# Kernel optimization log

Measured on AMD Instinct MI355X. Metric: run time of the kernel, lower is better.

The kernel has to match this reference:

```python
import jax, jax.numpy as jnp
import numpy as np
from jax import lax

B, CIN, COUT, H, W = 4, 256, 256, 64, 64
K = 3  # kernel size
PAD = 1
STRIDE = 1


def setup_inputs() -> dict:
    key = jax.random.key(0)
    k1, k2, k3, k4 = jax.random.split(key, 4)
    x = jax.random.normal(k1, (B, CIN, H, W), dtype=jnp.float32)
    # small offset weights so learned offsets are modest (original init is zeros)
    offset_w = jax.random.normal(k2, (3 * K * K, CIN, K, K), dtype=jnp.float32) * 0.01
    offset_b = jax.random.normal(k3, (3 * K * K,), dtype=jnp.float32) * 0.01
    dcn_w = jax.random.normal(k4, (COUT, CIN, K, K), dtype=jnp.float32) * (1.0 / np.sqrt(CIN * K * K))
    return {"x": x, "offset_w": offset_w, "offset_b": offset_b, "dcn_w": dcn_w}


def _dcnv2(x, offset_w, offset_b, dcn_w):
    b, c, h, w = x.shape
    kk = K * K
    # offset conv (standard 3x3, stride 1, pad 1)
    o = lax.conv_general_dilated(
        x, offset_w, (STRIDE, STRIDE), ((PAD, PAD), (PAD, PAD)),
        dimension_numbers=("NCHW", "OIHW", "NCHW"))
    o = o + offset_b[None, :, None, None]
    ho, wo = o.shape[2], o.shape[3]
    off = o[:, : 2 * kk].reshape(b, kk, 2, ho, wo)  # pairs are (dy, dx)
    dy, dx = off[:, :, 0], off[:, :, 1]             # [b,kk,ho,wo]
    mask = jax.nn.sigmoid(o[:, 2 * kk:])            # [b,kk,ho,wo]

    ki, kj = jnp.meshgrid(jnp.arange(K), jnp.arange(K), indexing="ij")
    ki = ki.reshape(kk).astype(jnp.float32)
    kj = kj.reshape(kk).astype(jnp.float32)
    base_y = (jnp.arange(ho, dtype=jnp.float32) * STRIDE - PAD)[None, None, :, None] + ki[None, :, None, None]
    base_x = (jnp.arange(wo, dtype=jnp.float32) * STRIDE - PAD)[None, None, None, :] + kj[None, :, None, None]
    py = base_y + dy  # [b,kk,ho,wo] sampling y
    px = base_x + dx  # sampling x

    y0 = jnp.floor(py)
    x0 = jnp.floor(px)
    wy = py - y0  # bilinear fractional weights
    wx = px - x0
    y0i = y0.astype(jnp.int32)
    x0i = x0.astype(jnp.int32)

    xT = x.transpose(0, 2, 3, 1)  # [b,h,w,c] for channel-last gathers
    bidx = jnp.arange(b)[:, None, None, None]

    def gather(yi, xi):
        # zero padding outside the image
        valid = (yi >= 0) & (yi < h) & (xi >= 0) & (xi < w)
        yc = jnp.clip(yi, 0, h - 1)
        xc = jnp.clip(xi, 0, w - 1)
        v = xT[bidx, yc, xc]  # [b,kk,ho,wo,c]
        return v * valid[..., None].astype(x.dtype)

    g00 = gather(y0i, x0i)
    g01 = gather(y0i, x0i + 1)
    g10 = gather(y0i + 1, x0i)
    g11 = gather(y0i + 1, x0i + 1)

    wy_ = wy[..., None]
    wx_ = wx[..., None]
    sampled = (g00 * (1 - wy_) * (1 - wx_) + g01 * (1 - wy_) * wx_
               + g10 * wy_ * (1 - wx_) + g11 * wy_ * wx_)
    sampled = sampled * mask[..., None]  # modulation

    wk = dcn_w.reshape(dcn_w.shape[0], c, kk)  # [o,c,kk]
    return jnp.einsum("bkhwc,ock->bohw", sampled, wk)


def reference(x, offset_w, offset_b, dcn_w):
    return _dcnv2(x, offset_w, offset_b, dcn_w)
```

## Files before the change

kernel.cpp:

```cpp
#include <hip/hip_runtime.h>
#include <hip/hip_bf16.h>
#include <stdint.h>
#include <math.h>

#define KDIM 2304

typedef __attribute__((ext_vector_type(8))) short bf16x8;
typedef __attribute__((ext_vector_type(4))) float f32x4;

__device__ inline unsigned short f2bf(float f) {
  union { float f; unsigned int u; } v; v.f = f;
  unsigned int u = v.u;
  unsigned int r = (u + 0x7FFFu + ((u >> 16) & 1u)) >> 16;
  return (unsigned short)r;
}
__device__ inline float bf2f(unsigned short h) {
  union { unsigned int u; float f; } v; v.u = ((unsigned int)h) << 16;
  return v.f;
}

__device__ inline void gl2lds16(const void* g, void* l) {
  __builtin_amdgcn_global_load_lds((const __attribute__((address_space(1))) void*)g,
                                   (__attribute__((address_space(3))) void*)l,
                                   16, 0, 0);
}

__global__ __launch_bounds__(256) void k_transpose(const float* __restrict__ x,
                                                   unsigned short* __restrict__ xTb) {
  __shared__ float tile[32][33];
  int t = threadIdx.x;
  int tx = t & 31, ty = t >> 5;
  int p0 = blockIdx.x * 32;
  int c0 = blockIdx.y * 32;
  int b  = blockIdx.z;
  const float* xb = x + ((size_t)b << 20);
#pragma unroll
  for (int i = 0; i < 4; ++i) {
    int c = c0 + ty + i * 8;
    tile[ty + i * 8][tx] = xb[((size_t)c << 12) + p0 + tx];
  }
  __syncthreads();
  unsigned short* ob = xTb + ((size_t)b << 20);
#pragma unroll
  for (int i = 0; i < 4; ++i) {
    int p = p0 + ty + i * 8;
    ob[(((size_t)p) << 8) + c0 + tx] = f2bf(tile[tx][ty + i * 8]);
  }
}

__global__ __launch_bounds__(256) void k_wprep(const float* __restrict__ dcn_w,
                                               const float* __restrict__ offset_w,
                                               unsigned short* __restrict__ Wpk,
                                               unsigned short* __restrict__ Wob,
                                               unsigned short* __restrict__ zp) {
  int gid = blockIdx.x * 256 + threadIdx.x;
  const int N1 = 72 * 8192;
  const int N2 = 32 * KDIM;
  if (gid < N1) {
    int j = gid & 7;
    int lane = (gid >> 3) & 63;
    int mb = (gid >> 9) & 15;
    int kc = gid >> 13;
    int row = mb * 16 + (lane & 15);
    int gk = kc * 32 + ((lane >> 4) << 3) + j;
    int c = gk & 255, kidx = gk >> 8;
    Wpk[gid] = f2bf(dcn_w[((size_t)(row * 256 + c)) * 9 + kidx]);
  } else if (gid < N1 + N2) {
    int g = gid - N1;
    int ch = g / KDIM, k = g % KDIM;
    int kidx = k >> 8, c = k & 255;
    Wob[g] = (ch < 27) ? f2bf(offset_w[((size_t)(ch * 256 + c)) * 9 + kidx])
                       : (unsigned short)0;
  } else if (gid < N1 + N2 + 128) {
    zp[gid - N1 - N2] = 0;
  }
}

__global__ __launch_bounds__(256) void k_offs_gemm(const unsigned short* __restrict__ xTb,
                                                   const unsigned short* __restrict__ Wob,
                                                   const unsigned short* __restrict__ zp,
                                                   float* __restrict__ O2p) {
  __shared__ unsigned short As[2][64 * 32];
  __shared__ unsigned short Bs[2][32 * 32];
  int t = threadIdx.x;
  int wv = t >> 6, lane = t & 63;
  int n0 = blockIdx.x * 64;
  int z = blockIdx.y;
  int r0 = t >> 2, coff = (t & 3) * 8;

  int rowA = n0 + r0;
  int b_ = rowA >> 12, hw = rowA & 4095, h = hw >> 6, w = hw & 63;

  f32x4 acc[2] = {};

  auto stage = [&](int kt, int buf) {
    int k0 = kt * 32;
    int kidx = k0 >> 8, c0 = k0 & 255;
    int di = kidx / 3 - 1, dj = kidx % 3 - 1;
    int y = h + di, xx = w + dj;
    const unsigned short* g = (y >= 0 && y < 64 && xx >= 0 && xx < 64)
        ? xTb + (((((size_t)b_) << 12) + (y << 6) + xx) << 8) + c0 + coff
        : zp;
    gl2lds16(g, (char*)As[buf] + wv * 1024);
    if (t < 128) {
      const unsigned short* gB = Wob + (size_t)(t >> 2) * KDIM + k0 + coff;
      gl2lds16(gB, (char*)Bs[buf] + wv * 1024);
    }
  };

  int kbeg = z * 36, kend = kbeg + 36;
  stage(kbeg, 0);

  for (int kt = kbeg; kt < kend; ++kt) {
    int buf = (kt - kbeg) & 1;
    if (kt + 1 < kend) {
      stage(kt + 1, buf ^ 1);
      if (wv < 2) asm volatile("s_waitcnt vmcnt(2)" ::: "memory");
      else        asm volatile("s_waitcnt vmcnt(1)" ::: "memory");
    } else {
      asm volatile("s_waitcnt vmcnt(0)" ::: "memory");
    }
    asm volatile("s_barrier" ::: "memory");

    bf16x8 aF, bF[2];
    aF = *(const bf16x8*)(As[buf] + (wv * 16 + (lane & 15)) * 32 + (lane >> 4) * 8);
#pragma unroll
    for (int j = 0; j < 2; ++j)
      bF[j] = *(const bf16x8*)(Bs[buf] + (j * 16 + (lane & 15)) * 32 + (lane >> 4) * 8);
#pragma unroll
    for (int j = 0; j < 2; ++j)
      acc[j] = __builtin_amdgcn_mfma_f32_16x16x32_bf16(aF, bF[j], acc[j], 0, 0, 0);

    asm volatile("s_barrier" ::: "memory");
  }

  int quad = lane >> 4, cl = lane & 15;
  float* O2z = O2p + (size_t)z * 16384 * 32;
#pragma unroll
  for (int j = 0; j < 2; ++j) {
    int col = j * 16 + cl;
#pragma unroll
    for (int r = 0; r < 4; ++r) {
      int row = n0 + wv * 16 + quad * 4 + r;
      O2z[(size_t)row * 32 + col] = acc[j][r];
    }
  }
}

__global__ __launch_bounds__(256) void k_sweights(const float* __restrict__ O2p,
                                                  const float* __restrict__ offb,
                                                  float* __restrict__ SW) {
  int gid = blockIdx.x * 256 + threadIdx.x;
  if (gid >= 9 * 16384) return;
  int k = gid >> 14;
  int bhw = gid & 16383;
  int h = (bhw >> 6) & 63, w = bhw & 63;

  const float* o0 = O2p + (size_t)bhw * 32;
  const float* o1 = o0 + (size_t)16384 * 32;
  float dy = o0[2 * k]     + o1[2 * k]     + offb[2 * k];
  float dx = o0[2 * k + 1] + o1[2 * k + 1] + offb[2 * k + 1];
  float mv = o0[18 + k]    + o1[18 + k]    + offb[18 + k];
  float mask = 1.0f / (1.0f + expf(-mv));

  float py = (float)(h - 1 + k / 3) + dy;
  float px = (float)(w - 1 + k % 3) + dx;
  float y0f = floorf(py), x0f = floorf(px);
  float wy = py - y0f, wx = px - x0f;
  int y0 = (int)y0f, x0 = (int)x0f;
  int y1 = y0 + 1, x1 = x0 + 1;

  float vy0 = (y0 >= 0 && y0 < 64) ? 1.f : 0.f;
  float vy1 = (y1 >= 0 && y1 < 64) ? 1.f : 0.f;
  float vx0 = (x0 >= 0 && x0 < 64) ? 1.f : 0.f;
  float vx1 = (x1 >= 0 && x1 < 64) ? 1.f : 0.f;
  int y0c = min(max(y0, 0), 63), y1c = min(max(y1, 0), 63);
  int x0c = min(max(x0, 0), 63), x1c = min(max(x1, 0), 63);

  float4 wv4;
  wv4.x = (1.f - wy) * (1.f - wx) * vy0 * vx0 * mask;
  wv4.y = (1.f - wy) * wx * vy0 * vx1 * mask;
  wv4.z = wy * (1.f - wx) * vy1 * vx0 * mask;
  wv4.w = wy * wx * vy1 * vx1 * mask;
  uint4 ov;
  ov.x = (unsigned)(((y0c << 6) + x0c) << 8);
  ov.y = (unsigned)(((y0c << 6) + x1c) << 8);
  ov.z = (unsigned)(((y1c << 6) + x0c) << 8);
  ov.w = (unsigned)(((y1c << 6) + x1c) << 8);

  float* p = SW + (size_t)gid * 8;
  *(float4*)p = wv4;
  *(uint4*)(p + 4) = ov;
}

__global__ __launch_bounds__(512) void k_fused(const unsigned short* __restrict__ Wpk,
                                               const unsigned short* __restrict__ xTb,
                                               const float* __restrict__ SW,
                                               float* __restrict__ out) {
  __shared__ __align__(16) unsigned short Bs[2][64 * 40];
  int t = threadIdx.x;
  int wv = t >> 6, lane = t & 63;
  int wm = wv & 3, wn = wv >> 2;
  int n0 = blockIdx.x * 64;
  int b  = n0 >> 12;
  const unsigned short* xb = xTb + ((size_t)b << 20);

  int r = t >> 3, g = t & 7;
  int ch0 = g * 4;
  int bsw = r * 40 + ch0;

  const unsigned short* wpBase = Wpk + ((size_t)(wm * 4 * 64 + lane)) * 8;

  f32x4 acc[4][2] = {};

  float4 wv4; uint4 ov;
  {
    const float* sw = SW + ((size_t)(n0 + r)) * 8;
    wv4 = *(const float4*)sw;
    ov  = *(const uint4*)(sw + 4);
  }
  float4 wv4n = wv4; uint4 ovn = ov;
  ushort4 q00, q01, q10, q11;
  bf16x8 aF[4], aFn[4];

  {
    unsigned c = (unsigned)ch0;
    q00 = *(const ushort4*)(xb + ov.x + c);
    q01 = *(const ushort4*)(xb + ov.y + c);
    q10 = *(const ushort4*)(xb + ov.z + c);
    q11 = *(const ushort4*)(xb + ov.w + c);
#pragma unroll
    for (int i = 0; i < 4; ++i)
      aF[i] = *(const bf16x8*)(wpBase + (size_t)i * 512);
  }

#pragma unroll 2
  for (int kt = 0; kt < 72; ++kt) {
    float s[4];
    s[0] = wv4.x * bf2f(q00.x) + wv4.y * bf2f(q01.x) + wv4.z * bf2f(q10.x) + wv4.w * bf2f(q11.x);
    s[1] = wv4.x * bf2f(q00.y) + wv4.y * bf2f(q01.y) + wv4.z * bf2f(q10.y) + wv4.w * bf2f(q11.y);
    s[2] = wv4.x * bf2f(q00.z) + wv4.y * bf2f(q01.z) + wv4.z * bf2f(q10.z) + wv4.w * bf2f(q11.z);
    s[3] = wv4.x * bf2f(q00.w) + wv4.y * bf2f(q01.w) + wv4.z * bf2f(q10.w) + wv4.w * bf2f(q11.w);
    union { __hip_bfloat162 h2[2]; ushort4 v; } pk;
    pk.h2[0] = __float22bfloat162_rn(make_float2(s[0], s[1]));
    pk.h2[1] = __float22bfloat162_rn(make_float2(s[2], s[3]));
    *(ushort4*)(&Bs[kt & 1][bsw]) = pk.v;

    if ((kt & 7) == 0 && kt < 64) {
      const float* swp = SW + ((size_t)((((kt >> 3) + 1) << 14) + n0 + r)) * 8;
      wv4n = *(const float4*)swp;
      ovn  = *(const uint4*)(swp + 4);
    }

    if (kt < 71) {
      int kn = kt + 1;
      if ((kn & 7) == 0) { wv4 = wv4n; ov = ovn; }
      unsigned c = (unsigned)(((kn & 7) << 5) + ch0);
      q00 = *(const ushort4*)(xb + ov.x + c);
      q01 = *(const ushort4*)(xb + ov.y + c);
      q10 = *(const ushort4*)(xb + ov.z + c);
      q11 = *(const ushort4*)(xb + ov.w + c);
#pragma unroll
      for (int i = 0; i < 4; ++i)
        aFn[i] = *(const bf16x8*)(wpBase + ((size_t)kn * 16 + i) * 512);
    }

    asm volatile("s_waitcnt lgkmcnt(0)\n\ts_barrier" ::: "memory");

    bf16x8 bF[2];
#pragma unroll
    for (int j = 0; j < 2; ++j)
      bF[j] = *(const bf16x8*)(&Bs[kt & 1][(wn * 32 + j * 16 + (lane & 15)) * 40 + (lane >> 4) * 8]);
#pragma unroll
    for (int i = 0; i < 4; ++i)
#pragma unroll
      for (int j = 0; j < 2; ++j)
        acc[i][j] = __builtin_amdgcn_mfma_f32_16x16x32_bf16(aF[i], bF[j], acc[i][j], 0, 0, 0);
    if (kt < 71) {
#pragma unroll
      for (int i = 0; i < 4; ++i) aF[i] = aFn[i];
    }
  }

  int quad = lane >> 4, cl = lane & 15;
  float* ob = out + (((size_t)b) << 20);
#pragma unroll
  for (int i = 0; i < 4; ++i) {
    int mbase = wm * 64 + i * 16 + quad * 4;
#pragma unroll
    for (int j = 0; j < 2; ++j) {
      int hw = (n0 & 4095) + wn * 32 + j * 16 + cl;
      float* op = ob + hw;
#pragma unroll
      for (int rr = 0; rr < 4; ++rr)
        op[((size_t)(mbase + rr)) << 12] = acc[i][j][rr];
    }
  }
}

extern "C" void kernel_launch(void* const* d_in, const int* in_sizes, int n_in,
                              void* d_out, int out_size, void* d_ws, size_t ws_size,
                              hipStream_t stream) {
  const float* x        = (const float*)d_in[0];
  const float* offset_w = (const float*)d_in[1];
  const float* offset_b = (const float*)d_in[2];
  const float* dcn_w    = (const float*)d_in[3];
  float* out = (float*)d_out;

  char* ws = (char*)d_ws;
  size_t off = 0;
  auto carve = [&](size_t bytes) -> void* {
    void* p = ws + off;
    off += (bytes + 255) & ~(size_t)255;
    return p;
  };
  unsigned short* xTb = (unsigned short*)carve(4ull * 64 * 64 * 256 * 2);
  unsigned short* Wpk = (unsigned short*)carve(72ull * 8192 * 2);
  unsigned short* Wob = (unsigned short*)carve(32ull * KDIM * 2);
  unsigned short* zp  = (unsigned short*)carve(256);
  float*          O2p = (float*)carve(2ull * 16384 * 32 * 4);
  float*          SW  = (float*)carve(9ull * 16384 * 8 * 4);
  (void)ws_size; (void)in_sizes; (void)n_in; (void)out_size;

  k_transpose<<<dim3(128, 8, 4), 256, 0, stream>>>(x, xTb);
  k_wprep<<<dim3((72 * 8192 + 32 * KDIM + 128 + 255) / 256), 256, 0, stream>>>(
      dcn_w, offset_w, Wpk, Wob, zp);
  k_offs_gemm<<<dim3(256, 2), 256, 0, stream>>>(xTb, Wob, zp, O2p);
  k_sweights<<<dim3((9 * 16384 + 255) / 256), 256, 0, stream>>>(O2p, offset_b, SW);
  k_fused<<<dim3(256), 512, 0, stream>>>(Wpk, xTb, SW, out);
}
```

Measured before the change: 156.1 us.

## Deepen fused DCN prefetch to two stages and swizzle block-to-tile mapping

The fused gather+GEMM loop is restructured into a manually unrolled pair of steps with two register sets, so the bilinear gather loads and weight fragments are prefetched two K-steps ahead instead of one. Each step issues its MFMAs before reloading its own A fragments, which shortens the dependency chain on memory latency. Both the offset GEMM and the fused kernel also remap blockIdx with a stride-32 swizzle to change which tiles run concurrently, for better cache locality. The cost is higher register pressure at 512 threads, and the wv4/ov switching logic becomes more delicate.

```diff
diff --git a/kernel.cpp b/kernel.cpp
--- a/kernel.cpp
+++ b/kernel.cpp
@@ -84,7 +84,9 @@
   __shared__ unsigned short Bs[2][32 * 32];
   int t = threadIdx.x;
   int wv = t >> 6, lane = t & 63;
-  int n0 = blockIdx.x * 64;
+  int bid = (int)blockIdx.x;
+  int swz = (bid & 7) * 32 + (bid >> 3);
+  int n0 = swz * 64;
   int z = blockIdx.y;
   int r0 = t >> 2, coff = (t & 3) * 8;
 
@@ -193,6 +195,57 @@
   *(uint4*)(p + 4) = ov;
 }
 
+#define FSTEP(KT, Q, AF, BUF, DOSW)                                            \
+  do {                                                                         \
+    float s0_ = wv4.x * bf2f(Q[0].x) + wv4.y * bf2f(Q[1].x) +                  \
+                wv4.z * bf2f(Q[2].x) + wv4.w * bf2f(Q[3].x);                   \
+    float s1_ = wv4.x * bf2f(Q[0].y) + wv4.y * bf2f(Q[1].y) +                  \
+                wv4.z * bf2f(Q[2].y) + wv4.w * bf2f(Q[3].y);                   \
+    float s2_ = wv4.x * bf2f(Q[0].z) + wv4.y * bf2f(Q[1].z) +                  \
+                wv4.z * bf2f(Q[2].z) + wv4.w * bf2f(Q[3].z);                   \
+    float s3_ = wv4.x * bf2f(Q[0].w) + wv4.y * bf2f(Q[1].w) +                  \
+                wv4.z * bf2f(Q[2].w) + wv4.w * bf2f(Q[3].w);                   \
+    union { __hip_bfloat162 h2[2]; ushort4 v; } pk_;                           \
+    pk_.h2[0] = __float22bfloat162_rn(make_float2(s0_, s1_));                  \
+    pk_.h2[1] = __float22bfloat162_rn(make_float2(s2_, s3_));                  \
+    *(ushort4*)(&Bs[BUF][bsw]) = pk_.v;                                        \
+    if (DOSW && ((KT) & 7) == 0 && (KT) < 64) {                                \
+      const float* swp_ =                                                      \
+          SW + ((size_t)(((((KT) >> 3) + 1) << 14) + n0 + r)) * 8;             \
+      wv4n = *(const float4*)swp_;                                             \
+      ovn  = *(const uint4*)(swp_ + 4);                                        \
+    }                                                                          \
+    if ((KT) < 70) {                                                           \
+      int kn_ = (KT) + 2;                                                      \
+      uint4 o_ = (((KT) & 7) >= 6) ? ovn : ov;                                 \
+      unsigned c_ = (unsigned)(((kn_ & 7) << 5) + ch0);                        \
+      Q[0] = *(const ushort4*)(xb + o_.x + c_);                                \
+      Q[1] = *(const ushort4*)(xb + o_.y + c_);                                \
+      Q[2] = *(const ushort4*)(xb + o_.z + c_);                                \
+      Q[3] = *(const ushort4*)(xb + o_.w + c_);                                \
+    }                                                                          \
+    asm volatile("s_waitcnt lgkmcnt(0)\n\ts_barrier" ::: "memory");            \
+    bf16x8 bF0_ = *(const bf16x8*)(&Bs[BUF][(wn * 32 + (lane & 15)) * 40 +     \
+                                            (lane >> 4) * 8]);                 \
+    bf16x8 bF1_ = *(const bf16x8*)(&Bs[BUF][(wn * 32 + 16 + (lane & 15)) * 40 +\
+                                            (lane >> 4) * 8]);                 \
+    _Pragma("unroll")                                                          \
+    for (int i_ = 0; i_ < 4; ++i_) {                                           \
+      acc[i_][0] =                                                             \
+          __builtin_amdgcn_mfma_f32_16x16x32_bf16(AF[i_], bF0_, acc[i_][0],    \
+                                                  0, 0, 0);                    \
+      acc[i_][1] =                                                             \
+          __builtin_amdgcn_mfma_f32_16x16x32_bf16(AF[i_], bF1_, acc[i_][1],    \
+                                                  0, 0, 0);                    \
+    }                                                                          \
+    if ((KT) < 70) {                                                           \
+      int kn_ = (KT) + 2;                                                      \
+      _Pragma("unroll")                                                        \
+      for (int i_ = 0; i_ < 4; ++i_)                                           \
+        AF[i_] = *(const bf16x8*)(wpBase + ((size_t)kn_ * 16 + i_) * 512);     \
+    }                                                                          \
+  } while (0)
+
 __global__ __launch_bounds__(512) void k_fused(const unsigned short* __restrict__ Wpk,
                                                const unsigned short* __restrict__ xTb,
                                                const float* __restrict__ SW,
@@ -201,7 +254,9 @@
   int t = threadIdx.x;
   int wv = t >> 6, lane = t & 63;
   int wm = wv & 3, wn = wv >> 2;
-  int n0 = blockIdx.x * 64;
+  int bid = (int)blockIdx.x;
+  int swz = (bid & 7) * 32 + (bid >> 3);
+  int n0 = swz * 64;
   int b  = n0 >> 12;
   const unsigned short* xb = xTb + ((size_t)b << 20);
 
@@ -213,73 +268,39 @@
 
   f32x4 acc[4][2] = {};
 
-  float4 wv4; uint4 ov;
+  float4 wv4, wv4n; uint4 ov, ovn;
   {
     const float* sw = SW + ((size_t)(n0 + r)) * 8;
     wv4 = *(const float4*)sw;
     ov  = *(const uint4*)(sw + 4);
   }
-  float4 wv4n = wv4; uint4 ovn = ov;
-  ushort4 q00, q01, q10, q11;
-  bf16x8 aF[4], aFn[4];
+  wv4n = wv4; ovn = ov;
+
+  ushort4 qA[4], qB[4];
+  bf16x8 aFA[4], aFB[4];
 
   {
-    unsigned c = (unsigned)ch0;
-    q00 = *(const ushort4*)(xb + ov.x + c);
-    q01 = *(const ushort4*)(xb + ov.y + c);
-    q10 = *(const ushort4*)(xb + ov.z + c);
-    q11 = *(const ushort4*)(xb + ov.w + c);
-#pragma unroll
-    for (int i = 0; i < 4; ++i)
-      aF[i] = *(const bf16x8*)(wpBase + (size_t)i * 512);
-  }
-
-#pragma unroll 2
-  for (int kt = 0; kt < 72; ++kt) {
-    float s[4];
-    s[0] = wv4.x * bf2f(q00.x) + wv4.y * bf2f(q01.x) + wv4.z * bf2f(q10.x) + wv4.w * bf2f(q11.x);
-    s[1] = wv4.x * bf2f(q00.y) + wv4.y * bf2f(q01.y) + wv4.z * bf2f(q10.y) + wv4.w * bf2f(q11.y);
-    s[2] = wv4.x * bf2f(q00.z) + wv4.y * bf2f(q01.z) + wv4.z * bf2f(q10.z) + wv4.w * bf2f(q11.z);
-    s[3] = wv4.x * bf2f(q00.w) + wv4.y * bf2f(q01.w) + wv4.z * bf2f(q10.w) + wv4.w * bf2f(q11.w);
-    union { __hip_bfloat162 h2[2]; ushort4 v; } pk;
-    pk.h2[0] = __float22bfloat162_rn(make_float2(s[0], s[1]));
-    pk.h2[1] = __float22bfloat162_rn(make_float2(s[2], s[3]));
-    *(ushort4*)(&Bs[kt & 1][bsw]) = pk.v;
-
-    if ((kt & 7) == 0 && kt < 64) {
-      const float* swp = SW + ((size_t)((((kt >> 3) + 1) << 14) + n0 + r)) * 8;
-      wv4n = *(const float4*)swp;
-      ovn  = *(const uint4*)(swp + 4);
-    }
-
-    if (kt < 71) {
-      int kn = kt + 1;
-      if ((kn & 7) == 0) { wv4 = wv4n; ov = ovn; }
-      unsigned c = (unsigned)(((kn & 7) << 5) + ch0);
-      q00 = *(const ushort4*)(xb + ov.x + c);
-      q01 = *(const ushort4*)(xb + ov.y + c);
-      q10 = *(const ushort4*)(xb + ov.z + c);
-      q11 = *(const ushort4*)(xb + ov.w + c);
-#pragma unroll
-      for (int i = 0; i < 4; ++i)
-        aFn[i] = *(const bf16x8*)(wpBase + ((size_t)kn * 16 + i) * 512);
-    }
-
-    asm volatile("s_waitcnt lgkmcnt(0)\n\ts_barrier" ::: "memory");
-
-    bf16x8 bF[2];
-#pragma unroll
-    for (int j = 0; j < 2; ++j)
-      bF[j] = *(const bf16x8*)(&Bs[kt & 1][(wn * 32 + j * 16 + (lane & 15)) * 40 + (lane >> 4) * 8]);
-#pragma unroll
-    for (int i = 0; i < 4; ++i)
-#pragma unroll
-      for (int j = 0; j < 2; ++j)
-        acc[i][j] = __builtin_amdgcn_mfma_f32_16x16x32_bf16(aF[i], bF[j], acc[i][j], 0, 0, 0);
-    if (kt < 71) {
-#pragma unroll
-      for (int i = 0; i < 4; ++i) aF[i] = aFn[i];
-    }
+    unsigned c0_ = (unsigned)ch0;
+    qA[0] = *(const ushort4*)(xb + ov.x + c0_);
+    qA[1] = *(const ushort4*)(xb + ov.y + c0_);
+    qA[2] = *(const ushort4*)(xb + ov.z + c0_);
+    qA[3] = *(const ushort4*)(xb + ov.w + c0_);
+    unsigned c1_ = (unsigned)(32 + ch0);
+    qB[0] = *(const ushort4*)(xb + ov.x + c1_);
+    qB[1] = *(const ushort4*)(xb + ov.y + c1_);
+    qB[2] = *(const ushort4*)(xb + ov.z + c1_);
+    qB[3] = *(const ushort4*)(xb + ov.w + c1_);
+#pragma unroll
+    for (int i = 0; i < 4; ++i) {
+      aFA[i] = *(const bf16x8*)(wpBase + (size_t)i * 512);
+      aFB[i] = *(const bf16x8*)(wpBase + (size_t)(16 + i) * 512);
+    }
+  }
+
+  for (int kt = 0; kt < 72; kt += 2) {
+    FSTEP(kt,     qA, aFA, 0, 1);
+    FSTEP(kt + 1, qB, aFB, 1, 0);
+    if ((kt & 7) == 6) { wv4 = wv4n; ov = ovn; }
   }
 
   int quad = lane >> 4, cl = lane & 15;
```

Result: faster. 149.6 us (-4.2%).
